# Performance work log

Hardware: AMD Instinct MI355X
Metric: run time of the kernel (lower is better)

The kernel has to match this reference:

```python
import jax, jax.numpy as jnp
import numpy as np

T, B, V, H = 512, 1024, 64, 100  # seq_len, batch, vocab(output_size), hidden_size


def setup_inputs() -> dict:
    key = jax.random.key(0)
    ks = jax.random.split(key, 9)
    s = 0.1
    x = jax.random.uniform(ks[0], (T, B, V), dtype=jnp.float32)  # teacher-forced inputs (one-hot-like floats)
    h = jax.random.normal(ks[1], (1, B, H), dtype=jnp.float32)   # encoder final hidden
    lens = jax.random.randint(ks[2], (B,), 1, T + 1, dtype=jnp.int32)
    lengths = jnp.sort(lens)[::-1]          # descending, packed-sequence order
    lengths = lengths.at[0].set(T)          # max length == T (batch_sizes[0] == B)
    W_ih = jax.random.normal(ks[3], (3 * H, V), dtype=jnp.float32) * s
    W_hh = jax.random.normal(ks[4], (3 * H, H), dtype=jnp.float32) * s
    b_ih = jax.random.normal(ks[5], (3 * H,), dtype=jnp.float32) * s
    b_hh = jax.random.normal(ks[6], (3 * H,), dtype=jnp.float32) * s
    W_out = jax.random.normal(ks[7], (V, H), dtype=jnp.float32) * s
    b_out = jax.random.normal(ks[8], (V,), dtype=jnp.float32) * s
    return dict(x=x, h=h, lengths=lengths, W_ih=W_ih, W_hh=W_hh,
                b_ih=b_ih, b_hh=b_hh, W_out=W_out, b_out=b_out)


def gru_cell(x_t, h_t, W_ih, W_hh, b_ih, b_hh):
    # PyTorch nn.GRUCell math, gate order (r, z, n)
    gi = x_t @ W_ih.T + b_ih   # [B, 3H]
    gh = h_t @ W_hh.T + b_hh   # [B, 3H]
    i_r, i_z, i_n = jnp.split(gi, 3, axis=-1)
    h_r, h_z, h_n = jnp.split(gh, 3, axis=-1)
    r = jax.nn.sigmoid(i_r + h_r)
    z = jax.nn.sigmoid(i_z + h_z)
    n = jnp.tanh(i_n + r * h_n)
    return (1.0 - z) * n + z * h_t


def reference(x, h, lengths, W_ih, W_hh, b_ih, b_hh, W_out, b_out):
    # Packed-sequence GRUCell decode with full teacher forcing (forcing_ratio=1.0).
    # Padded emulation: at step t only rows with t < length are active
    # (== first batch_sizes[t] rows in packed order since lengths are descending).
    hidden0 = h[0]                                          # [B, H]
    mask = jnp.arange(T)[:, None] < lengths[None, :]        # [T, B]

    def step(hidden, inp):
        x_t, m = inp
        h_new = gru_cell(x_t, hidden, W_ih, W_hh, b_ih, b_hh)
        hidden = jnp.where(m[:, None], h_new, hidden)
        logp = jax.nn.log_softmax(hidden @ W_out.T + b_out, axis=-1)  # [B, V]
        return hidden, jnp.where(m[:, None], logp, 0.0)

    _, outputs = jax.lax.scan(step, hidden0, (x, mask))
    return outputs  # [T, B, V] log-probs, zero at padded positions
```

## Files before the change

### kernel.cpp

```cpp
#include <hip/hip_runtime.h>


#define T_STEPS 512
#define BATCH   1024
#define VOCAB   64
#define HID     100
#define BB      16
#define NKH     4
#define HSTR    136
#define XSTR    72

typedef _Float16 f16;
typedef _Float16 f16x8 __attribute__((ext_vector_type(8)));
typedef float    f32x4 __attribute__((ext_vector_type(4)));

#define MFMA(A_, B_, C_) __builtin_amdgcn_mfma_f32_16x16x32_f16((A_), (B_), (C_), 0, 0, 0)

__device__ __forceinline__ float rcp_f(float v)  { return __builtin_amdgcn_rcpf(v); }
__device__ __forceinline__ float sigm(float v)   { return rcp_f(1.0f + __expf(-v)); }
__device__ __forceinline__ float tanh_f(float v) { return 1.0f - 2.0f * rcp_f(__expf(2.0f * v) + 1.0f); }

template<int CTRL>
__device__ __forceinline__ float dpp_mov(float v) {
    return __int_as_float(__builtin_amdgcn_update_dpp(
        0, __float_as_int(v), CTRL, 0xF, 0xF, true));
}
__device__ __forceinline__ float red_max16(float v) {
    v = fmaxf(v, dpp_mov<0xB1>(v));
    v = fmaxf(v, dpp_mov<0x4E>(v));
    v = fmaxf(v, dpp_mov<0x141>(v));
    v = fmaxf(v, dpp_mov<0x140>(v));
    return v;
}
__device__ __forceinline__ float red_sum16(float v) {
    v += dpp_mov<0xB1>(v);
    v += dpp_mov<0x4E>(v);
    v += dpp_mov<0x141>(v);
    v += dpp_mov<0x140>(v);
    return v;
}

__device__ __forceinline__ void sync_lds() {
    __builtin_amdgcn_sched_barrier(0);
    asm volatile("s_waitcnt lgkmcnt(0)" ::: "memory");
    __builtin_amdgcn_s_barrier();
    __builtin_amdgcn_sched_barrier(0);
}

#define HLOADX(P0, P1, P2, P3, tt) do {                                     \
    const float* xp_ = x + ((size_t)(tt) * BATCH + rowbase + xrow) * VOCAB + xcol; \
    P0 = *reinterpret_cast<const float4*>(xp_);                             \
    P1 = *reinterpret_cast<const float4*>(xp_ + 4);                         \
    P2 = *reinterpret_cast<const float4*>(xp_ + 8);                         \
    P3 = *reinterpret_cast<const float4*>(xp_ + 12);                        \
} while (0)
#define HSTAGEX(P0, P1, P2, P3, buf) do {                                   \
    f16x8 a_, b_;                                                           \
    a_[0]=(f16)P0.x; a_[1]=(f16)P0.y; a_[2]=(f16)P0.z; a_[3]=(f16)P0.w;     \
    a_[4]=(f16)P1.x; a_[5]=(f16)P1.y; a_[6]=(f16)P1.z; a_[7]=(f16)P1.w;     \
    b_[0]=(f16)P2.x; b_[1]=(f16)P2.y; b_[2]=(f16)P2.z; b_[3]=(f16)P2.w;     \
    b_[4]=(f16)P3.x; b_[5]=(f16)P3.y; b_[6]=(f16)P3.z; b_[7]=(f16)P3.w;     \
    *reinterpret_cast<f16x8*>(&xs[buf][xrow][xcol])     = a_;               \
    *reinterpret_cast<f16x8*>(&xs[buf][xrow][xcol + 8]) = b_;               \
} while (0)

__global__ __launch_bounds__(512, 2) void gru_mfma(
    const float* __restrict__ x, const float* __restrict__ h0,
    const int* __restrict__ lengths,
    const float* __restrict__ W_ih, const float* __restrict__ W_hh,
    const float* __restrict__ b_ih, const float* __restrict__ b_hh,
    const float* __restrict__ W_out, const float* __restrict__ b_out,
    float* __restrict__ out)
{
    const int tid = threadIdx.x;
    const int w   = tid >> 6;
    const int l   = tid & 63;
    const int c   = l & 15;
    const int lg  = l >> 4;
    const int rowbase = blockIdx.x * BB;

    __shared__ alignas(16) f16 hHi[2][BB * HSTR];
    __shared__ alignas(16) f16 hLo[2][BB * HSTR];
    __shared__ alignas(16) f16 xs[2][BB][XSTR];

    f16x8 wf[18];
    float bin = 0.f;
    float hold4[4];
    int   lenv[4];

    #pragma unroll
    for (int r = 0; r < 4; ++r) lenv[r] = lengths[rowbase + lg * 4 + r];

    if (w < 7) {
        const int gl = 16 * w + c;
        const bool gv = gl < HID;
        #pragma unroll
        for (int s = 0; s < 3; ++s) {
            const int g = s * HID + gl;
            #pragma unroll
            for (int ks = 0; ks < NKH; ++ks) {
                f16x8 v;
                #pragma unroll
                for (int j = 0; j < 8; ++j) {
                    const int k = ks * 32 + lg * 8 + j;
                    float val = 0.f;
                    if (gv) {
                        if (k < HID)        val = W_hh[(size_t)g * HID + k];
                        else if (k == HID)  val = (s < 2) ? (b_ih[g] + b_hh[g]) : b_hh[g];
                    }
                    v[j] = (f16)val;
                }
                wf[s * 4 + ks] = v;
            }
            #pragma unroll
            for (int ks = 0; ks < 2; ++ks) {
                f16x8 v;
                #pragma unroll
                for (int j = 0; j < 8; ++j) {
                    const int k = ks * 32 + lg * 8 + j;
                    v[j] = (f16)(gv ? W_ih[(size_t)g * VOCAB + k] : 0.f);
                }
                wf[12 + s * 2 + ks] = v;
            }
        }
        bin = gv ? b_ih[2 * HID + gl] : 0.f;

        #pragma unroll
        for (int r = 0; r < 4; ++r) {
            const int row = lg * 4 + r;
            float hv = gv ? h0[(size_t)(rowbase + row) * HID + gl] : 0.f;
            hold4[r] = hv;
            if (gv) {
                f16 hi = (f16)hv;
                hHi[0][row * HSTR + gl] = hi;
                hLo[0][row * HSTR + gl] = (f16)(hv - (float)hi);
            }
        }
    } else {
        #pragma unroll
        for (int vt = 0; vt < 4; ++vt) {
            const int vr = 16 * vt + c;
            #pragma unroll
            for (int ks = 0; ks < NKH; ++ks) {
                f16x8 v;
                #pragma unroll
                for (int j = 0; j < 8; ++j) {
                    const int k = ks * 32 + lg * 8 + j;
                    float val = 0.f;
                    if (k < HID)        val = W_out[(size_t)vr * HID + k];
                    else if (k == HID)  val = b_out[vr];
                    v[j] = (f16)val;
                }
                wf[vt * 4 + ks] = v;
            }
        }
        hold4[0] = hold4[1] = hold4[2] = hold4[3] = 0.f;
    }

    if (tid < BB) {
        #pragma unroll
        for (int k = HID; k < 128; ++k) {
            hHi[0][tid * HSTR + k] = (f16)0.f;  hLo[0][tid * HSTR + k] = (f16)0.f;
            hHi[1][tid * HSTR + k] = (f16)0.f;  hLo[1][tid * HSTR + k] = (f16)0.f;
        }
        hHi[0][tid * HSTR + HID] = (f16)1.0f;
        hHi[1][tid * HSTR + HID] = (f16)1.0f;
    }

    const int xrow = l >> 2;
    const int xcol = (l & 3) * 16;
    float4 qA0, qA1, qA2, qA3, qB0, qB1, qB2, qB3;
    if (w == 7) {
        HLOADX(qA0, qA1, qA2, qA3, 0);
        HSTAGEX(qA0, qA1, qA2, qA3, 0);
        HLOADX(qA0, qA1, qA2, qA3, 1);
        HLOADX(qB0, qB1, qB2, qB3, 2);
    }
    __syncthreads();

    for (int t = 0; t <= T_STEPS; ++t) {
        const int cur = t & 1;
        if (w < 7) {
            if (t < T_STEPS) {
                f16x8 xq0 = *reinterpret_cast<const f16x8*>(&xs[cur][c][lg * 8]);
                f16x8 xq1 = *reinterpret_cast<const f16x8*>(&xs[cur][c][32 + lg * 8]);
                f16x8 hh[NKH], hl[NKH];
                #pragma unroll
                for (int ks = 0; ks < NKH; ++ks) {
                    const int off = c * HSTR + ks * 32 + lg * 8;
                    hh[ks] = *reinterpret_cast<const f16x8*>(&hHi[cur][off]);
                    hl[ks] = *reinterpret_cast<const f16x8*>(&hLo[cur][off]);
                }

                f32x4 zz = {0.f, 0.f, 0.f, 0.f};
                f32x4 aRa = zz, aZa = zz, aNX = zz;
                f32x4 aRb = zz, aZb = zz, aNHa = zz, aNHb = zz;
                __builtin_amdgcn_s_setprio(1);
                aRa = MFMA(xq0, wf[12], aRa);
                aZa = MFMA(xq0, wf[14], aZa);
                aNX = MFMA(xq0, wf[16], aNX);
                aRa = MFMA(xq1, wf[13], aRa);
                aZa = MFMA(xq1, wf[15], aZa);
                aNX = MFMA(xq1, wf[17], aNX);
                #pragma unroll
                for (int ks = 0; ks < NKH; ++ks) {
                    aRa  = MFMA(hh[ks], wf[0 + ks], aRa);
                    aRb  = MFMA(hl[ks], wf[0 + ks], aRb);
                    aZa  = MFMA(hh[ks], wf[4 + ks], aZa);
                    aZb  = MFMA(hl[ks], wf[4 + ks], aZb);
                    aNHa = MFMA(hh[ks], wf[8 + ks], aNHa);
                    aNHb = MFMA(hl[ks], wf[8 + ks], aNHb);
                }
                __builtin_amdgcn_s_setprio(0);

                const int kk = 16 * w + c;
                const bool kv = kk < HID;
                #pragma unroll
                for (int r = 0; r < 4; ++r) {
                    float rg   = sigm(aRa[r] + aRb[r]);
                    float zg   = sigm(aZa[r] + aZb[r]);
                    float ng   = tanh_f(fmaf(rg, aNHa[r] + aNHb[r], aNX[r] + bin));
                    float hnew = fmaf(zg, hold4[r] - ng, ng);
                    float hv   = (t < lenv[r]) ? hnew : hold4[r];
                    hold4[r] = hv;
                    if (kv) {
                        const int row = lg * 4 + r;
                        f16 hi = (f16)hv;
                        hHi[cur ^ 1][row * HSTR + kk] = hi;
                        hLo[cur ^ 1][row * HSTR + kk] = (f16)(hv - (float)hi);
                    }
                }
            }
        } else {
            if (t < T_STEPS) {
                const int tt = (t + 3 < T_STEPS) ? t + 3 : T_STEPS - 1;
                if ((t & 1) == 0) {
                    HSTAGEX(qA0, qA1, qA2, qA3, 1);
                    HLOADX(qA0, qA1, qA2, qA3, tt);
                } else {
                    HSTAGEX(qB0, qB1, qB2, qB3, 0);
                    HLOADX(qB0, qB1, qB2, qB3, tt);
                }
            }
            if (t > 0) {
                const int tp = t - 1;
                f16x8 hh[NKH];
                #pragma unroll
                for (int ks = 0; ks < NKH; ++ks) {
                    const int off = c * HSTR + ks * 32 + lg * 8;
                    hh[ks] = *reinterpret_cast<const f16x8*>(&hHi[cur][off]);
                }
                f32x4 zz = {0.f, 0.f, 0.f, 0.f};
                f32x4 a0 = zz, a1 = zz, a2 = zz, a3 = zz;
                #pragma unroll
                for (int ks = 0; ks < NKH; ++ks) {
                    a0 = MFMA(hh[ks], wf[0  + ks], a0);
                    a1 = MFMA(hh[ks], wf[4  + ks], a1);
                    a2 = MFMA(hh[ks], wf[8  + ks], a2);
                    a3 = MFMA(hh[ks], wf[12 + ks], a3);
                }
                #pragma unroll
                for (int r = 0; r < 4; ++r) {
                    float v0 = a0[r], v1 = a1[r], v2 = a2[r], v3 = a3[r];
                    float m = red_max16(fmaxf(fmaxf(v0, v1), fmaxf(v2, v3)));
                    float s = red_sum16(__expf(v0 - m) + __expf(v1 - m)
                                      + __expf(v2 - m) + __expf(v3 - m));
                    float ls = m + __logf(s);
                    const bool act = tp < lenv[r];
                    float* orow = out + ((size_t)tp * BATCH + rowbase + lg * 4 + r) * VOCAB + c;
                    orow[ 0] = act ? (v0 - ls) : 0.f;
                    orow[16] = act ? (v1 - ls) : 0.f;
                    orow[32] = act ? (v2 - ls) : 0.f;
                    orow[48] = act ? (v3 - ls) : 0.f;
                }
            }
        }
        sync_lds();
    }
}

extern "C" void kernel_launch(void* const* d_in, const int* in_sizes, int n_in,
                              void* d_out, int out_size, void* d_ws, size_t ws_size,
                              hipStream_t stream) {
    const float* x     = (const float*)d_in[0];
    const float* h0    = (const float*)d_in[1];
    const int*   lens  = (const int*)  d_in[2];
    const float* W_ih  = (const float*)d_in[3];
    const float* W_hh  = (const float*)d_in[4];
    const float* b_ih  = (const float*)d_in[5];
    const float* b_hh  = (const float*)d_in[6];
    const float* W_out = (const float*)d_in[7];
    const float* b_out = (const float*)d_in[8];
    float* outp = (float*)d_out;

    gru_mfma<<<BATCH / BB, 512, 0, stream>>>(x, h0, lens, W_ih, W_hh,
                                             b_ih, b_hh, W_out, b_out, outp);
}
```

Baseline: 903.9 us.

## Shrink per-block batch rows to two to spread the recurrence across more CUs

Cuts the batch rows handled per block from 16 to 2, so the grid grows eightfold and occupies far more compute units. The MFMA tiles stay 16 rows wide, with the unused rows zero-padded in LDS. Only lane group 0 publishes hidden state and writes outputs. Occupancy is raised to 4 blocks per SIMD set, and the n-gate input bias is folded into the accumulator initial value. The sequential per-step latency chain and the MFMA count per block do not change, so blocks sharing a CU may contend, and most MFMA work is spent on padding.

```diff
diff --git a/kernel.cpp b/kernel.cpp
--- a/kernel.cpp
+++ b/kernel.cpp
@@ -5,7 +5,7 @@
 #define BATCH   1024
 #define VOCAB   64
 #define HID     100
-#define BB      16
+#define BB      2
 #define NKH     4
 #define HSTR    136
 #define XSTR    72
@@ -64,7 +64,7 @@
     *reinterpret_cast<f16x8*>(&xs[buf][xrow][xcol + 8]) = b_;               \
 } while (0)
 
-__global__ __launch_bounds__(512, 2) void gru_mfma(
+__global__ __launch_bounds__(512, 4) void gru_mfma(
     const float* __restrict__ x, const float* __restrict__ h0,
     const int* __restrict__ lengths,
     const float* __restrict__ W_ih, const float* __restrict__ W_hh,
@@ -79,17 +79,17 @@
     const int lg  = l >> 4;
     const int rowbase = blockIdx.x * BB;
 
-    __shared__ alignas(16) f16 hHi[2][BB * HSTR];
-    __shared__ alignas(16) f16 hLo[2][BB * HSTR];
-    __shared__ alignas(16) f16 xs[2][BB][XSTR];
+    __shared__ alignas(16) f16 hHi[2][16 * HSTR];
+    __shared__ alignas(16) f16 hLo[2][16 * HSTR];
+    __shared__ alignas(16) f16 xs[2][16][XSTR];
 
     f16x8 wf[18];
     float bin = 0.f;
-    float hold4[4];
-    int   lenv[4];
+    float hold[BB];
+    int   lenv[BB];
 
     #pragma unroll
-    for (int r = 0; r < 4; ++r) lenv[r] = lengths[rowbase + lg * 4 + r];
+    for (int r = 0; r < BB; ++r) lenv[r] = lengths[rowbase + r];
 
     if (w < 7) {
         const int gl = 16 * w + c;
@@ -126,14 +126,13 @@
         bin = gv ? b_ih[2 * HID + gl] : 0.f;
 
         #pragma unroll
-        for (int r = 0; r < 4; ++r) {
-            const int row = lg * 4 + r;
-            float hv = gv ? h0[(size_t)(rowbase + row) * HID + gl] : 0.f;
-            hold4[r] = hv;
-            if (gv) {
+        for (int r = 0; r < BB; ++r) {
+            float hv = (gv && lg == 0) ? h0[(size_t)(rowbase + r) * HID + gl] : 0.f;
+            hold[r] = hv;
+            if (gv && lg == 0) {
                 f16 hi = (f16)hv;
-                hHi[0][row * HSTR + gl] = hi;
-                hLo[0][row * HSTR + gl] = (f16)(hv - (float)hi);
+                hHi[0][r * HSTR + gl] = hi;
+                hLo[0][r * HSTR + gl] = (f16)(hv - (float)hi);
             }
         }
     } else {
@@ -154,23 +153,32 @@
                 wf[vt * 4 + ks] = v;
             }
         }
-        hold4[0] = hold4[1] = hold4[2] = hold4[3] = 0.f;
+        #pragma unroll
+        for (int r = 0; r < BB; ++r) hold[r] = 0.f;
     }
 
-    if (tid < BB) {
-        #pragma unroll
-        for (int k = HID; k < 128; ++k) {
-            hHi[0][tid * HSTR + k] = (f16)0.f;  hLo[0][tid * HSTR + k] = (f16)0.f;
-            hHi[1][tid * HSTR + k] = (f16)0.f;  hLo[1][tid * HSTR + k] = (f16)0.f;
-        }
-        hHi[0][tid * HSTR + HID] = (f16)1.0f;
-        hHi[1][tid * HSTR + HID] = (f16)1.0f;
+    if (tid < 16) {
+        const int row = tid;
+        const int k0 = (row < BB) ? HID : 0;
+        for (int k = k0; k < 128; ++k) {
+            hHi[0][row * HSTR + k] = (f16)0.f;  hLo[0][row * HSTR + k] = (f16)0.f;
+            hHi[1][row * HSTR + k] = (f16)0.f;  hLo[1][row * HSTR + k] = (f16)0.f;
+        }
+        if (row < BB) {
+            hHi[0][row * HSTR + HID] = (f16)1.0f;
+            hHi[1][row * HSTR + HID] = (f16)1.0f;
+        } else {
+            for (int k = 0; k < VOCAB; ++k) {
+                xs[0][row][k] = (f16)0.f;
+                xs[1][row][k] = (f16)0.f;
+            }
+        }
     }
 
     const int xrow = l >> 2;
     const int xcol = (l & 3) * 16;
     float4 qA0, qA1, qA2, qA3, qB0, qB1, qB2, qB3;
-    if (w == 7) {
+    if (w == 7 && xrow < BB) {
         HLOADX(qA0, qA1, qA2, qA3, 0);
         HSTAGEX(qA0, qA1, qA2, qA3, 0);
         HLOADX(qA0, qA1, qA2, qA3, 1);
@@ -193,7 +201,8 @@
                 }
 
                 f32x4 zz = {0.f, 0.f, 0.f, 0.f};
-                f32x4 aRa = zz, aZa = zz, aNX = zz;
+                f32x4 aRa = zz, aZa = zz;
+                f32x4 aNX = {bin, bin, bin, bin};
                 f32x4 aRb = zz, aZb = zz, aNHa = zz, aNHb = zz;
                 __builtin_amdgcn_s_setprio(1);
                 aRa = MFMA(xq0, wf[12], aRa);
@@ -214,25 +223,24 @@
                 __builtin_amdgcn_s_setprio(0);
 
                 const int kk = 16 * w + c;
-                const bool kv = kk < HID;
-                #pragma unroll
-                for (int r = 0; r < 4; ++r) {
+                const bool pub = (kk < HID) && (lg == 0);
+                #pragma unroll
+                for (int r = 0; r < BB; ++r) {
                     float rg   = sigm(aRa[r] + aRb[r]);
                     float zg   = sigm(aZa[r] + aZb[r]);
-                    float ng   = tanh_f(fmaf(rg, aNHa[r] + aNHb[r], aNX[r] + bin));
-                    float hnew = fmaf(zg, hold4[r] - ng, ng);
-                    float hv   = (t < lenv[r]) ? hnew : hold4[r];
-                    hold4[r] = hv;
-                    if (kv) {
-                        const int row = lg * 4 + r;
+                    float ng   = tanh_f(fmaf(rg, aNHa[r] + aNHb[r], aNX[r]));
+                    float hnew = fmaf(zg, hold[r] - ng, ng);
+                    float hv   = (t < lenv[r]) ? hnew : hold[r];
+                    hold[r] = hv;
+                    if (pub) {
                         f16 hi = (f16)hv;
-                        hHi[cur ^ 1][row * HSTR + kk] = hi;
-                        hLo[cur ^ 1][row * HSTR + kk] = (f16)(hv - (float)hi);
+                        hHi[cur ^ 1][r * HSTR + kk] = hi;
+                        hLo[cur ^ 1][r * HSTR + kk] = (f16)(hv - (float)hi);
                     }
                 }
             }
         } else {
-            if (t < T_STEPS) {
+            if (t < T_STEPS && xrow < BB) {
                 const int tt = (t + 3 < T_STEPS) ? t + 3 : T_STEPS - 1;
                 if ((t & 1) == 0) {
                     HSTAGEX(qA0, qA1, qA2, qA3, 1);
@@ -260,18 +268,20 @@
                     a3 = MFMA(hh[ks], wf[12 + ks], a3);
                 }
                 #pragma unroll
-                for (int r = 0; r < 4; ++r) {
+                for (int r = 0; r < BB; ++r) {
                     float v0 = a0[r], v1 = a1[r], v2 = a2[r], v3 = a3[r];
                     float m = red_max16(fmaxf(fmaxf(v0, v1), fmaxf(v2, v3)));
                     float s = red_sum16(__expf(v0 - m) + __expf(v1 - m)
                                       + __expf(v2 - m) + __expf(v3 - m));
                     float ls = m + __logf(s);
-                    const bool act = tp < lenv[r];
-                    float* orow = out + ((size_t)tp * BATCH + rowbase + lg * 4 + r) * VOCAB + c;
-                    orow[ 0] = act ? (v0 - ls) : 0.f;
-                    orow[16] = act ? (v1 - ls) : 0.f;
-                    orow[32] = act ? (v2 - ls) : 0.f;
-                    orow[48] = act ? (v3 - ls) : 0.f;
+                    if (lg == 0) {
+                        const bool act = tp < lenv[r];
+                        float* orow = out + ((size_t)tp * BATCH + rowbase + r) * VOCAB + c;
+                        orow[ 0] = act ? (v0 - ls) : 0.f;
+                        orow[16] = act ? (v1 - ls) : 0.f;
+                        orow[32] = act ? (v2 - ls) : 0.f;
+                        orow[48] = act ? (v3 - ls) : 0.f;
+                    }
                 }
             }
         }
```

Measured after the change: 1.514 ms. 67.5% more time.
